# Kernel tuning notes

Hardware: AMD Instinct MI355X
Metric: run time of the kernel (lower is better)

The kernel has to match this reference:

```python
import jax, jax.numpy as jnp
import numpy as np

HIDDEN = 64
NUM_LAYERS = 6
BN_EPS = 1e-5


def setup_inputs() -> dict:
    key = jax.random.key(0)
    N, M = 1024, 1024
    num_nodes = N + M
    ks = jax.random.split(key, 12)
    x = jax.random.normal(ks[0], (num_nodes, 2), dtype=jnp.float32)
    # complete bipartite edges: (a, N+b) for all a in [0,N), b in [0,M), row-major so view(N,M) is meaningful
    row = jnp.repeat(jnp.arange(N, dtype=jnp.int64), M)
    col = N + jnp.tile(jnp.arange(M, dtype=jnp.int64), N)
    edge_index = jnp.stack([row, col], axis=0)
    s = 1.0 / np.sqrt(HIDDEN)
    return {
        "x": x,
        "edge_index": edge_index,
        "in_w": jax.random.normal(ks[1], (2, HIDDEN), jnp.float32) * 0.5,
        "in_b": jnp.zeros((HIDDEN,), jnp.float32),
        "conv_w": jax.random.normal(ks[2], (NUM_LAYERS, HIDDEN, HIDDEN), jnp.float32) * s,
        "conv_b": jnp.zeros((NUM_LAYERS, HIDDEN), jnp.float32),
        "bn_gamma": jnp.ones((NUM_LAYERS, HIDDEN), jnp.float32),
        "bn_beta": jnp.zeros((NUM_LAYERS, HIDDEN), jnp.float32),
        "out_w": jax.random.normal(ks[3], (2 * HIDDEN, 1), jnp.float32) * s,
        "out_b": jnp.zeros((1,), jnp.float32),
        "N": N,
        "M": M,
    }


def reference(x, edge_index, in_w, in_b, conv_w, conv_b, bn_gamma, bn_beta, out_w, out_b, N, M):
    num_nodes = x.shape[0]
    # GCN normalization with added self-loops (PyG GCNConv defaults)
    loops = jnp.arange(num_nodes, dtype=edge_index.dtype)
    row = jnp.concatenate([edge_index[0], loops])
    col = jnp.concatenate([edge_index[1], loops])
    deg = jax.ops.segment_sum(jnp.ones_like(col, dtype=x.dtype), col, num_segments=num_nodes)
    dinv = jnp.where(deg > 0, jax.lax.rsqrt(deg), 0.0)
    norm = dinv[row] * dinv[col]  # [E+num_nodes]

    h = jax.nn.relu(x @ in_w + in_b)
    for i in range(NUM_LAYERS):
        h_res = h
        hw = h @ conv_w[i]
        agg = jax.ops.segment_sum(hw[row] * norm[:, None], col, num_segments=num_nodes)
        h = agg + conv_b[i]
        # BatchNorm1d in training mode: batch stats, biased variance
        mu = h.mean(axis=0)
        var = ((h - mu) ** 2).mean(axis=0)
        h = (h - mu) * jax.lax.rsqrt(var + BN_EPS) * bn_gamma[i] + bn_beta[i]
        h = jax.nn.relu(h)
        if i > 0 and i % 2 == 1:
            h = h + h_res

    ef = jnp.concatenate([h[edge_index[0]], h[edge_index[1]]], axis=1)  # [E, 2H]
    scores = (ef @ out_w + out_b)[:, 0]
    return scores.reshape(N, M)
```

## Files before the change

kernel.cpp:

```cpp
#include <hip/hip_runtime.h>


#define NBLK 64
#define MAGIC 0x13572468u

__device__ __forceinline__ float relu_(float x) { return x > 0.f ? x : 0.f; }

#define AT_LOAD(p)    __hip_atomic_load((p), __ATOMIC_RELAXED, __HIP_MEMORY_SCOPE_AGENT)
#define AT_STORE(p,v) __hip_atomic_store((p), (v), __ATOMIC_RELAXED, __HIP_MEMORY_SCOPE_AGENT)
#define AT_ADD(p,v)   __hip_atomic_fetch_add((p), (v), __ATOMIC_RELAXED, __HIP_MEMORY_SCOPE_AGENT)

#define PART_OFF  256
#define UV_OFF    12544
#define FLAG_OFF  14592

__global__ __launch_bounds__(256, 1) void k_fused(
    const float* __restrict__ x,
    const float* __restrict__ in_w, const float* __restrict__ in_b,
    const float* __restrict__ conv_w,
    const float* __restrict__ bn_g, const float* __restrict__ bn_b,
    const float* __restrict__ out_w, const float* __restrict__ out_b,
    float* __restrict__ out,
    unsigned int* __restrict__ ws)
{
    __shared__ float hl[32 * 68];
    __shared__ float sredS[4 * 64], sredQ[4 * 64];
    __shared__ float pcoef[64], scoef[64];
    __shared__ float u_l[16];

    const int t = threadIdx.x, b = blockIdx.x;
    const int nl = t >> 3;
    const int fi = t & 7;
    const int f0 = fi * 8;
    const int node = b * 32 + nl;
    const bool isA = b < 32;
    float* part = (float*)(ws + PART_OFF);
    float* uv   = (float*)(ws + UV_OFF);

    if (b == 0) {
        for (int i = t; i < 224; i += 256) AT_STORE(ws + i, 0u);
        for (int i = t; i < 12288; i += 256) AT_STORE((unsigned*)part + i, 0u);
        asm volatile("s_waitcnt vmcnt(0)" ::: "memory");
        __syncthreads();
        if (t == 0) AT_STORE(ws + FLAG_OFF, MAGIC);
    }

    {
        float x0 = x[node * 2], x1 = x[node * 2 + 1];
#pragma unroll
        for (int j = 0; j < 8; j++) {
            int f = f0 + j;
            hl[nl * 68 + f] = relu_(fmaf(x0, in_w[f], fmaf(x1, in_w[64 + f], in_b[f])));
        }
    }
    __syncthreads();

    for (int layer = 0; layer < 6; layer++) {
        const float* W = conv_w + layer * 4096;
        float acc[8];
#pragma unroll
        for (int j = 0; j < 8; j++) acc[j] = 0.f;

#pragma unroll 4
        for (int k = 0; k < 64; k += 4) {
            float4 hh = *(const float4*)&hl[nl * 68 + k];
            float hv[4] = {hh.x, hh.y, hh.z, hh.w};
#pragma unroll
            for (int j = 0; j < 4; j++) {
                const float* wr = W + (k + j) * 64 + f0;
                float4 w0 = *(const float4*)wr;
                float4 w1 = *(const float4*)(wr + 4);
                float wv[8] = {w0.x, w0.y, w0.z, w0.w, w1.x, w1.y, w1.z, w1.w};
#pragma unroll
                for (int q = 0; q < 8; q++) acc[q] = fmaf(hv[j], wv[q], acc[q]);
            }
        }

        {
            float sv[8], qv[8];
#pragma unroll
            for (int j = 0; j < 8; j++) { sv[j] = acc[j]; qv[j] = acc[j] * acc[j]; }
#pragma unroll
            for (int m = 8; m < 64; m <<= 1) {
#pragma unroll
                for (int j = 0; j < 8; j++) {
                    sv[j] += __shfl_xor(sv[j], m);
                    qv[j] += __shfl_xor(qv[j], m);
                }
            }
            int w = t >> 6, lane = t & 63;
            if (lane < 8) {
#pragma unroll
                for (int j = 0; j < 8; j++) {
                    sredS[w * 64 + lane * 8 + j] = sv[j];
                    sredQ[w * 64 + lane * 8 + j] = qv[j];
                }
            }
        }
        if (layer == 0) {
            __syncthreads();
            if (t == 0) while (AT_LOAD(ws + FLAG_OFF) != MAGIC) {}
        }
        __syncthreads();

        if (t < 64) {
            float S = sredS[t] + sredS[64 + t] + sredS[128 + t] + sredS[192 + t];
            float Q = sredQ[t] + sredQ[64 + t] + sredQ[128 + t] + sredQ[192 + t];
            float* base = part + layer * 2048 + (b & 7) * 256 + (isA ? 0 : 128);
            AT_ADD(base + t, S);
            AT_ADD(base + 64 + t, Q);
        }

        asm volatile("s_waitcnt vmcnt(0)" ::: "memory");
        __syncthreads();
        if (t == 0) {
            unsigned int* c = ws + layer * 32;
            AT_ADD(c, 1u);
            for (;;) {
                unsigned a0 = AT_LOAD(c);
                unsigned a1 = AT_LOAD(c);
                unsigned a2 = AT_LOAD(c);
                unsigned a3 = AT_LOAD(c);
                if (a0 >= NBLK) break;
                if (a1 >= NBLK) break;
                if (a2 >= NBLK) break;
                if (a3 >= NBLK) break;
            }
        }
        __syncthreads();

        if (t < 64) {
            const float* base = part + layer * 2048;
            float SA = 0.f, QA = 0.f, SB = 0.f, QB = 0.f;
#pragma unroll
            for (int r = 0; r < 8; r++) {
                const float* rb = base + r * 256;
                SA += AT_LOAD(rb + t);
                QA += AT_LOAD(rb + 64 + t);
                SB += AT_LOAD(rb + 128 + t);
                QB += AT_LOAD(rb + 192 + t);
            }
            const float c1 = 9.75609756097561e-4f;
            const float c2 = 3.1234752377721214e-2f;
            float sumAgg = SA + c1 * SB + 1024.f * c2 * SA;
            float sumSq  = QA + c1 * c1 * QB + 2.f * c1 * c2 * SA * SB
                         + 1024.f * c2 * c2 * SA * SA;
            float meanAgg = sumAgg * (1.f / 2048.f);
            float var = sumSq * (1.f / 2048.f) - meanAgg * meanAgg;
            float rstd = rsqrtf(var + 1e-5f);
            float scale = rstd * bn_g[layer * 64 + t];
            float bt = bn_b[layer * 64 + t];
            if (isA) { pcoef[t] = scale;      scoef[t] = bt - meanAgg * scale; }
            else     { pcoef[t] = c1 * scale; scoef[t] = bt + (c2 * SA - meanAgg) * scale; }
        }
        __syncthreads();

        float vals[8];
#pragma unroll
        for (int j = 0; j < 8; j++)
            vals[j] = relu_(fmaf(acc[j], pcoef[f0 + j], scoef[f0 + j]));
        if (layer == 1 || layer == 3 || layer == 5) {
#pragma unroll
            for (int j = 0; j < 8; j++) vals[j] += hl[nl * 68 + f0 + j];
        }

        if (layer < 5) {
#pragma unroll
            for (int j = 0; j < 8; j++) hl[nl * 68 + f0 + j] = vals[j];
            __syncthreads();
        } else {
            const float* w = out_w + (isA ? 0 : 64) + f0;
            float d = 0.f;
#pragma unroll
            for (int j = 0; j < 8; j++) d = fmaf(vals[j], w[j], d);
            d += __shfl_xor(d, 1);
            d += __shfl_xor(d, 2);
            d += __shfl_xor(d, 4);
            if (fi == 0) AT_STORE(uv + node, d);
        }
    }

    asm volatile("s_waitcnt vmcnt(0)" ::: "memory");
    __syncthreads();
    if (t == 0) {
        unsigned int* c = ws + 6 * 32;
        AT_ADD(c, 1u);
        for (;;) {
            unsigned a0 = AT_LOAD(c);
            unsigned a1 = AT_LOAD(c);
            unsigned a2 = AT_LOAD(c);
            unsigned a3 = AT_LOAD(c);
            if (a0 >= NBLK) break;
            if (a1 >= NBLK) break;
            if (a2 >= NBLK) break;
            if (a3 >= NBLK) break;
        }
    }
    __syncthreads();

    {
        if (t < 16) u_l[t] = AT_LOAD(uv + b * 16 + t);
        float ob = out_b[0];
        float4 vv;
        vv.x = AT_LOAD(uv + 1024 + 4 * t)     + ob;
        vv.y = AT_LOAD(uv + 1024 + 4 * t + 1) + ob;
        vv.z = AT_LOAD(uv + 1024 + 4 * t + 2) + ob;
        vv.w = AT_LOAD(uv + 1024 + 4 * t + 3) + ob;
        __syncthreads();
#pragma unroll
        for (int r = 0; r < 16; r++) {
            int a = b * 16 + r;
            float ua = u_l[r];
            ((float4*)(out + a * 1024))[t] =
                make_float4(ua + vv.x, ua + vv.y, ua + vv.z, ua + vv.w);
        }
    }
}

extern "C" void kernel_launch(void* const* d_in, const int* in_sizes, int n_in,
                              void* d_out, int out_size, void* d_ws, size_t ws_size,
                              hipStream_t stream) {
    const float* x      = (const float*)d_in[0];
    const float* in_w   = (const float*)d_in[2];
    const float* in_b   = (const float*)d_in[3];
    const float* conv_w = (const float*)d_in[4];
    const float* bn_g   = (const float*)d_in[6];
    const float* bn_b   = (const float*)d_in[7];
    const float* out_w  = (const float*)d_in[8];
    const float* out_b  = (const float*)d_in[9];
    float* out = (float*)d_out;

    k_fused<<<NBLK, 256, 0, stream>>>(x, in_w, in_b, conv_w, bn_g, bn_b,
                                      out_w, out_b, out, (unsigned int*)d_ws);
}
```

Measured before the change: 124.9 us.

## Stage conv weights in LDS with double-buffered prefetch during grid barrier

Conv weights are now staged in shared memory. The next layer's weights are prefetched into registers while each block waits at the inter-block barrier, then written to the alternate LDS buffer. BN gamma/beta and the output weights are also cached in LDS. The goal is to take global-memory weight reads out of the per-layer matvec and hide their latency behind barrier spin time. The cost is roughly 36KB of extra LDS plus extra registers.

```diff
diff --git a/kernel.cpp b/kernel.cpp
--- a/kernel.cpp
+++ b/kernel.cpp
@@ -23,9 +23,12 @@
     float* __restrict__ out,
     unsigned int* __restrict__ ws)
 {
+    __shared__ float Wl[2][4096];
     __shared__ float hl[32 * 68];
     __shared__ float sredS[4 * 64], sredQ[4 * 64];
     __shared__ float pcoef[64], scoef[64];
+    __shared__ float g_lds[384], b_lds[384];
+    __shared__ float ow_lds[128];
     __shared__ float u_l[16];
 
     const int t = threadIdx.x, b = blockIdx.x;
@@ -37,6 +40,17 @@
     float* part = (float*)(ws + PART_OFF);
     float* uv   = (float*)(ws + UV_OFF);
 
+    {
+        const float4* src = (const float4*)conv_w;
+        float4* dst = (float4*)Wl[0];
+        dst[t]       = src[t];
+        dst[t + 256] = src[t + 256];
+        dst[t + 512] = src[t + 512];
+        dst[t + 768] = src[t + 768];
+        for (int i = t; i < 384; i += 256) { g_lds[i] = bn_g[i]; b_lds[i] = bn_b[i]; }
+        if (t < 128) ow_lds[t] = out_w[t];
+    }
+
     if (b == 0) {
         for (int i = t; i < 224; i += 256) AT_STORE(ws + i, 0u);
         for (int i = t; i < 12288; i += 256) AT_STORE((unsigned*)part + i, 0u);
@@ -56,7 +70,7 @@
     __syncthreads();
 
     for (int layer = 0; layer < 6; layer++) {
-        const float* W = conv_w + layer * 4096;
+        const float* Wb = Wl[layer & 1];
         float acc[8];
 #pragma unroll
         for (int j = 0; j < 8; j++) acc[j] = 0.f;
@@ -67,7 +81,7 @@
             float hv[4] = {hh.x, hh.y, hh.z, hh.w};
 #pragma unroll
             for (int j = 0; j < 4; j++) {
-                const float* wr = W + (k + j) * 64 + f0;
+                const float* wr = Wb + (k + j) * 64 + f0;
                 float4 w0 = *(const float4*)wr;
                 float4 w1 = *(const float4*)(wr + 4);
                 float wv[8] = {w0.x, w0.y, w0.z, w0.w, w1.x, w1.y, w1.z, w1.w};
@@ -113,9 +127,19 @@
 
         asm volatile("s_waitcnt vmcnt(0)" ::: "memory");
         __syncthreads();
+        if (t == 0) AT_ADD(ws + layer * 32, 1u);
+
+        float4 pf0, pf1, pf2, pf3;
+        if (layer < 5) {
+            const float4* src = (const float4*)(conv_w + (layer + 1) * 4096);
+            pf0 = src[t];
+            pf1 = src[t + 256];
+            pf2 = src[t + 512];
+            pf3 = src[t + 768];
+        }
+
         if (t == 0) {
-            unsigned int* c = ws + layer * 32;
-            AT_ADD(c, 1u);
+            const unsigned int* c = ws + layer * 32;
             for (;;) {
                 unsigned a0 = AT_LOAD(c);
                 unsigned a1 = AT_LOAD(c);
@@ -129,6 +153,14 @@
         }
         __syncthreads();
 
+        if (layer < 5) {
+            float4* dst = (float4*)Wl[(layer + 1) & 1];
+            dst[t]       = pf0;
+            dst[t + 256] = pf1;
+            dst[t + 512] = pf2;
+            dst[t + 768] = pf3;
+        }
+
         if (t < 64) {
             const float* base = part + layer * 2048;
             float SA = 0.f, QA = 0.f, SB = 0.f, QB = 0.f;
@@ -148,8 +180,8 @@
             float meanAgg = sumAgg * (1.f / 2048.f);
             float var = sumSq * (1.f / 2048.f) - meanAgg * meanAgg;
             float rstd = rsqrtf(var + 1e-5f);
-            float scale = rstd * bn_g[layer * 64 + t];
-            float bt = bn_b[layer * 64 + t];
+            float scale = rstd * g_lds[layer * 64 + t];
+            float bt = b_lds[layer * 64 + t];
             if (isA) { pcoef[t] = scale;      scoef[t] = bt - meanAgg * scale; }
             else     { pcoef[t] = c1 * scale; scoef[t] = bt + (c2 * SA - meanAgg) * scale; }
         }
@@ -169,7 +201,7 @@
             for (int j = 0; j < 8; j++) hl[nl * 68 + f0 + j] = vals[j];
             __syncthreads();
         } else {
-            const float* w = out_w + (isA ? 0 : 64) + f0;
+            const float* w = ow_lds + (isA ? 0 : 64) + f0;
             float d = 0.f;
 #pragma unroll
             for (int j = 0; j < 8; j++) d = fmaf(vals[j], w[j], d);
```

Result: faster. 115.7 us (-7.4%).
